# Kernel tuning notes

Hardware: AMD Instinct MI355X
Metric: run time of the kernel (lower is better)

Reference implementation:

```python
import jax, jax.numpy as jnp
import numpy as np
import math

N_LAYER = 3
D = 256
NH = 4
MULT = 128
N = MULT * D // NH  # 8192
VOCAB = 256
EPS = 1e-5
TWO_PI = 2.0 * math.pi


def _get_freqs(n, theta=2.0 ** 16):
    t = jnp.arange(0, n, dtype=jnp.float32)
    q = jnp.floor(t / 2.0) * 2.0  # quantize to pairs
    return 1.0 / (theta ** (q / n)) / TWO_PI  # [N]


def _ln(x):
    # LayerNorm over last dim, no affine
    mu = jnp.mean(x, axis=-1, keepdims=True)
    var = jnp.var(x, axis=-1, keepdims=True)
    return (x - mu) / jnp.sqrt(var + EPS)


def _rope(phases, v):
    # phases: [T, N] (cycles); v: [..., T, N]
    ph = (phases % 1.0) * TWO_PI
    c, s = jnp.cos(ph), jnp.sin(ph)
    v_rot = jnp.stack((-v[..., 1::2], v[..., ::2]), axis=-1).reshape(v.shape)
    return v * c + v_rot * s


def setup_inputs() -> dict:
    key = jax.random.key(0)
    ks = jax.random.split(key, 6)
    B, T = 1, 1024
    std = 0.02
    return {
        "idx": jax.random.randint(ks[0], (B, T), 0, VOCAB),
        "embed": jax.random.normal(ks[1], (VOCAB, D), jnp.float32) * std,
        "encoder": jax.random.normal(ks[2], (NH, D, N), jnp.float32) * std,
        "encoder_v": jax.random.normal(ks[3], (NH, D, N), jnp.float32) * std,
        "decoder": jax.random.normal(ks[4], (NH * N, D), jnp.float32) * std,
        "lm_head": jax.random.normal(ks[5], (D, VOCAB), jnp.float32) * std,
    }


def reference(idx, embed, encoder, encoder_v, decoder, lm_head):
    B, T = idx.shape
    freqs = _get_freqs(N)  # [N]
    phases = jnp.arange(T, dtype=jnp.float32)[:, None] * freqs[None, :]  # [T, N]
    # strict lower triangular causal mask (diagonal excluded)
    causal = jnp.tril(jnp.ones((T, T), dtype=jnp.bool_), k=-1)

    x = _ln(embed[idx])  # [B, T, D]
    for _ in range(N_LAYER):
        # encoder projection + ReLU sparsification: [B, nh, T, N]
        x_sparse = jax.nn.relu(jnp.einsum('btd,hdn->bhtn', x, encoder))
        # RoPE on Q (= K)
        qr = _rope(phases, x_sparse)
        # unnormalized bilinear causal attention (no softmax)
        scores = jnp.einsum('bhtn,bhsn->bhts', qr, qr)
        scores = jnp.where(causal, scores, 0.0)
        ykv = _ln(jnp.einsum('bhts,bsd->bhtd', scores, x))  # [B, nh, T, D]
        y_sparse = jax.nn.relu(jnp.einsum('bhtd,hdn->bhtn', ykv, encoder_v))
        xy = x_sparse * y_sparse  # [B, nh, T, N]
        # MLP decode: head-major flatten of (nh, N) matches decoder rows
        ymlp = jnp.einsum('bhtn,btd... wrong', xy) if False else (
            xy.transpose(0, 2, 1, 3).reshape(B, T, NH * N) @ decoder)  # [B, T, D]
        x = _ln(x + _ln(ymlp))
    logits = x @ lm_head  # [B, T, VOCAB]
    return logits
```

## Files before the change

### kernel.cpp

```cpp
#include <hip/hip_runtime.h>
#include <hip/hip_bf16.h>
#include <math.h>
#include <stdint.h>

#define T_SEQ 1024
#define D_DIM 256
#define NH_C 4
#define N_DIM 8192
#define VOCAB_C 256
#define NLAYER 3
#define TWO_PI_F 6.283185307179586f
#define KSPLIT_DEC 16
#define KSPLIT_SC 4

typedef __bf16 bf16x8 __attribute__((ext_vector_type(8)));
typedef float f32x4 __attribute__((ext_vector_type(4)));

__device__ __forceinline__ unsigned short f2bf(float f) {
  unsigned u = __builtin_bit_cast(unsigned, f);
  u += 0x7fffu + ((u >> 16) & 1u);
  return (unsigned short)(u >> 16);
}
__device__ __forceinline__ float bf2f(unsigned short h) {
  unsigned u = ((unsigned)h) << 16;
  return __builtin_bit_cast(float, u);
}
__device__ __forceinline__ unsigned pack2(float a, float b) {
  return (unsigned)f2bf(a) | ((unsigned)f2bf(b) << 16);
}

typedef __attribute__((address_space(3))) uint32_t lds_u32;
typedef __attribute__((address_space(1))) const uint32_t glob_u32;
__device__ __forceinline__ void gload_lds16(const void* g, void* l) {
  __builtin_amdgcn_global_load_lds(reinterpret_cast<glob_u32*>(reinterpret_cast<uintptr_t>(g)),
                                   reinterpret_cast<lds_u32*>(reinterpret_cast<uintptr_t>(l)), 16, 0,
                                   0);
}

__global__ void k_transpose(const float* __restrict__ src, unsigned short* __restrict__ dst,
                            int R, int C, long sB, long dB) {
  __shared__ float tile[32][33];
  const int b = blockIdx.z;
  src += (size_t)b * sB;
  dst += (size_t)b * dB;
  const int c0 = blockIdx.x * 32, r0 = blockIdx.y * 32;
  const int tx = threadIdx.x, ty = threadIdx.y;
#pragma unroll
  for (int i = 0; i < 32; i += 8)
    tile[ty + i][tx] = src[(size_t)(r0 + ty + i) * C + (c0 + tx)];
  __syncthreads();
#pragma unroll
  for (int i = 0; i < 32; i += 8)
    dst[(size_t)(c0 + ty + i) * R + (r0 + tx)] = f2bf(tile[tx][ty + i]);
}

__global__ void k_ropetab(unsigned* __restrict__ cs) {
  const int id = blockIdx.x * 256 + threadIdx.x;
  const int pair = id >> 10, t = id & 1023;
  const float freq = exp2f(-(float)pair * (1.0f / 256.0f)) * (1.0f / TWO_PI_F);
  float ph = (float)t * freq;
  ph -= floorf(ph);
  float s, c;
  __sincosf(ph * TWO_PI_F, &s, &c);
  cs[id] = pack2(c, s);
}

__device__ __forceinline__ void stats256(float4 v, float& mu, float& rs) {
  float s = v.x + v.y + v.z + v.w;
  float ss = v.x * v.x + v.y * v.y + v.z * v.z + v.w * v.w;
#pragma unroll
  for (int o = 1; o < 64; o <<= 1) { s += __shfl_xor(s, o); ss += __shfl_xor(ss, o); }
  mu = s * (1.0f / 256.0f);
  float var = ss * (1.0f / 256.0f) - mu * mu;
  rs = rsqrtf(var + 1e-5f);
}

__global__ void k_embed_ln(const int* __restrict__ idx, const float* __restrict__ embed,
                           float* __restrict__ x, unsigned short* __restrict__ xb,
                           unsigned short* __restrict__ xT) {
  const int t = blockIdx.x, lane = threadIdx.x;
  const float* row = embed + (size_t)idx[t] * D_DIM;
  float4 v = ((const float4*)row)[lane];
  float mu, rs;
  stats256(v, mu, rs);
  float4 o = make_float4((v.x - mu) * rs, (v.y - mu) * rs, (v.z - mu) * rs, (v.w - mu) * rs);
  ((float4*)(x + (size_t)t * D_DIM))[lane] = o;
  ((uint2*)(xb + (size_t)t * D_DIM))[lane] = make_uint2(pack2(o.x, o.y), pack2(o.z, o.w));
  const int d0 = lane * 4;
  xT[(size_t)(d0 + 0) * T_SEQ + t] = f2bf(o.x);
  xT[(size_t)(d0 + 1) * T_SEQ + t] = f2bf(o.y);
  xT[(size_t)(d0 + 2) * T_SEQ + t] = f2bf(o.z);
  xT[(size_t)(d0 + 3) * T_SEQ + t] = f2bf(o.w);
}

__global__ void k_ln_rows(const float* __restrict__ in, unsigned short* __restrict__ outb) {
  const int r = blockIdx.x, lane = threadIdx.x;
  float4 v = ((const float4*)(in + (size_t)r * D_DIM))[lane];
  float mu, rs;
  stats256(v, mu, rs);
  ((uint2*)(outb + (size_t)r * D_DIM))[lane] =
      make_uint2(pack2((v.x - mu) * rs, (v.y - mu) * rs), pack2((v.z - mu) * rs, (v.w - mu) * rs));
}

template <int NP>
__global__ void k_update_x(const float* __restrict__ ymlp, float* __restrict__ x,
                           unsigned short* __restrict__ xb, unsigned short* __restrict__ xT) {
  const int t = blockIdx.x, lane = threadIdx.x;
  float4 m = make_float4(0.f, 0.f, 0.f, 0.f);
#pragma unroll
  for (int pp = 0; pp < NP; ++pp) {
    float4 q = ((const float4*)(ymlp + (size_t)pp * T_SEQ * D_DIM + (size_t)t * D_DIM))[lane];
    m.x += q.x; m.y += q.y; m.z += q.z; m.w += q.w;
  }
  float mu1, rs1;
  stats256(m, mu1, rs1);
  float4 xv = ((const float4*)(x + (size_t)t * D_DIM))[lane];
  float4 z = make_float4(xv.x + (m.x - mu1) * rs1, xv.y + (m.y - mu1) * rs1,
                         xv.z + (m.z - mu1) * rs1, xv.w + (m.w - mu1) * rs1);
  float mu2, rs2;
  stats256(z, mu2, rs2);
  float4 o = make_float4((z.x - mu2) * rs2, (z.y - mu2) * rs2, (z.z - mu2) * rs2, (z.w - mu2) * rs2);
  ((float4*)(x + (size_t)t * D_DIM))[lane] = o;
  ((uint2*)(xb + (size_t)t * D_DIM))[lane] = make_uint2(pack2(o.x, o.y), pack2(o.z, o.w));
  const int d0 = lane * 4;
  xT[(size_t)(d0 + 0) * T_SEQ + t] = f2bf(o.x);
  xT[(size_t)(d0 + 1) * T_SEQ + t] = f2bf(o.y);
  xT[(size_t)(d0 + 2) * T_SEQ + t] = f2bf(o.z);
  xT[(size_t)(d0 + 3) * T_SEQ + t] = f2bf(o.w);
}

template <int NP>
__global__ void k_comb(const float* __restrict__ sp, unsigned short* __restrict__ sc) {
  const size_t gid = (size_t)blockIdx.x * 256 + threadIdx.x;
  const size_t e0 = gid * 8;
  const int s = (int)(e0 & (T_SEQ - 1));
  const int t = (int)((e0 >> 10) & (T_SEQ - 1));
  if (s >= t) return;
  const int h = (int)(e0 >> 20);
  float v[8] = {0.f, 0.f, 0.f, 0.f, 0.f, 0.f, 0.f, 0.f};
#pragma unroll
  for (int pp = 0; pp < NP; ++pp) {
    const float* a = sp + ((size_t)(h * NP + pp)) * T_SEQ * T_SEQ + (size_t)t * T_SEQ + s;
    float4 a0 = *(const float4*)a, a1 = *(const float4*)(a + 4);
    v[0] += a0.x; v[1] += a0.y; v[2] += a0.z; v[3] += a0.w;
    v[4] += a1.x; v[5] += a1.y; v[6] += a1.z; v[7] += a1.w;
  }
  unsigned short o[8];
#pragma unroll
  for (int j = 0; j < 8; ++j) o[j] = (s + j < t) ? f2bf(v[j]) : (unsigned short)0;
  *(uint4*)(sc + e0) = *(uint4*)o;
}

template <int MODE, int BM, int BN, bool TRI_A>
__global__ __launch_bounds__(256) void k_gemm(const unsigned short* __restrict__ A, long lda, long sAz,
                                              const unsigned short* __restrict__ B, long ldb, long sBz,
                                              void* __restrict__ Cv, long ldc, long sCz,
                                              const unsigned short* __restrict__ extra, long sEz,
                                              unsigned short* __restrict__ C2,
                                              const unsigned* __restrict__ ctab, int Ksize) {
  constexpr int MF = BM / 32;
  constexpr int NF = BN / 32;
  constexpr int BUFB = (BM + BN) * 128;

  const unsigned nbx = gridDim.x, nby = gridDim.y;
  const unsigned total = nbx * nby * gridDim.z;
  const unsigned lid = (blockIdx.z * nby + blockIdx.y) * nbx + blockIdx.x;
  const unsigned qq = total >> 3, rr = total & 7;
  const unsigned xcd = lid & 7, loc = lid >> 3;
  const unsigned wg = (xcd < rr ? xcd * (qq + 1) : rr * (qq + 1) + (xcd - rr) * qq) + loc;
  const int bx = wg % nbx;
  const int by = (wg / nbx) % nby;
  const int bz = wg / (nbx * nby);

  const int i0 = by * BM;
  const int j0 = bx * BN;
  if ((MODE == 2 || MODE == 6) && j0 >= i0 + BM) return;

  int zAB = bz, kbase = 0;
  if constexpr (MODE == 7) kbase = bz * Ksize;
  if constexpr (MODE == 6) { zAB = bz >> 2; kbase = (bz & (KSPLIT_SC - 1)) * Ksize; }
  A += (size_t)zAB * sAz;
  B += (size_t)zAB * sBz;
  float* Cf = (float*)Cv + (size_t)bz * sCz;
  unsigned short* Ch = (unsigned short*)Cv + (size_t)bz * sCz;
  unsigned short* C2h = C2 ? C2 + (size_t)bz * sCz : nullptr;
  const unsigned short* E = extra ? extra + (size_t)bz * sEz : nullptr;

  const int tid = threadIdx.x;
  const int lane = tid & 63, w = tid >> 6;
  const int wr = w >> 1, wc = w & 1;

  __shared__ __align__(16) char lds[2 * BUFB];

  f32x4 acc[MF][NF];
#pragma unroll
  for (int m = 0; m < MF; ++m)
#pragma unroll
    for (int n = 0; n < NF; ++n) acc[m][n] = f32x4{0.f, 0.f, 0.f, 0.f};

  const char* Abytes = (const char*)A;
  const char* Bbytes = (const char*)B;
  const size_t ldab = (size_t)((MODE == 7) ? N_DIM : lda) * 2;
  const size_t ldbb = (size_t)ldb * 2;
  const int lr = lane >> 3;
  const int scol = ((lane & 7) * 16) ^ (lr << 4);

  auto stage = [&](int buf, int kt) {
    const int kk = kbase + kt * 64;
    const char* Ag;
    if constexpr (MODE == 7) {
      Ag = Abytes +
           ((size_t)(kk >> 13) * ((size_t)T_SEQ * N_DIM) + (size_t)i0 * N_DIM + (kk & (N_DIM - 1))) * 2;
    } else {
      Ag = Abytes + ((size_t)i0 * lda + kk) * 2;
    }
    const char* Bg = Bbytes + ((size_t)j0 * ldb + kk) * 2;
    char* lb = lds + buf * BUFB;
#pragma unroll
    for (int it = 0; it < BM / 32; ++it) {
      const int r0 = (w + 4 * it) * 8;
      gload_lds16(Ag + (size_t)(r0 + lr) * ldab + scol, lb + r0 * 128);
    }
#pragma unroll
    for (int it = 0; it < BN / 32; ++it) {
      const int r0 = (w + 4 * it) * 8;
      gload_lds16(Bg + (size_t)(r0 + lr) * ldbb + scol, lb + BM * 128 + r0 * 128);
    }
  };

  const int ar = lane & 15;
  const int ko16 = (lane >> 4) * 16;
  const int swz = (lane & 7) << 4;

  auto compute = [&](const char* Ab) {
    const char* Bb = Ab + BM * 128;
    bf16x8 af[2][MF], bfr[2][NF];
#pragma unroll
    for (int kk = 0; kk < 2; ++kk) {
      const int koff = (kk * 64 + ko16) ^ swz;
#pragma unroll
      for (int m = 0; m < MF; ++m)
        af[kk][m] = *(const bf16x8*)(Ab + (size_t)(wr * (BM / 2) + m * 16 + ar) * 128 + koff);
#pragma unroll
      for (int n = 0; n < NF; ++n)
        bfr[kk][n] = *(const bf16x8*)(Bb + (size_t)(wc * (BN / 2) + n * 16 + ar) * 128 + koff);
    }
#pragma unroll
    for (int kk = 0; kk < 2; ++kk)
#pragma unroll
      for (int m = 0; m < MF; ++m)
#pragma unroll
        for (int n = 0; n < NF; ++n)
          acc[m][n] = __builtin_amdgcn_mfma_f32_16x16x32_bf16(af[kk][m], bfr[kk][n], acc[m][n], 0, 0, 0);
  };

  const int nt = TRI_A ? (i0 / 64 + BM / 64) : Ksize / 64;
  stage(0, 0);
  __syncthreads();
  int cur = 0;
  for (int t = 0; t < nt; ++t) {
    if (t + 1 < nt) stage(cur ^ 1, t + 1);
    compute(lds + cur * BUFB);
    __syncthreads();
    cur ^= 1;
  }

#pragma unroll
  for (int m = 0; m < MF; ++m) {
    const int row0 = i0 + wr * (BM / 2) + m * 16 + ((lane >> 4) << 2);
#pragma unroll
    for (int n = 0; n < NF; ++n) {
      const int col = j0 + wc * (BN / 2) + n * 16 + (lane & 15);
      f32x4 c = acc[m][n];
      if constexpr (MODE == 4) {
        const uint4 q = *(const uint4*)(ctab + (size_t)(col >> 1) * T_SEQ + row0);
        const unsigned qw[4] = {q.x, q.y, q.z, q.w};
        const float sgn = (lane & 1) ? 1.f : -1.f;
#pragma unroll
        for (int r = 0; r < 4; ++r) {
          const float v = fmaxf(c[r], 0.f);
          const float pv = __shfl_xor(v, 1);
          const float cc = bf2f((unsigned short)(qw[r] & 0xffffu));
          const float ss = bf2f((unsigned short)(qw[r] >> 16));
          Ch[(size_t)(row0 + r) * ldc + col] = f2bf(v);
          C2h[(size_t)(row0 + r) * ldc + col] = f2bf(v * cc + sgn * pv * ss);
        }
      } else {
#pragma unroll
        for (int r = 0; r < 4; ++r) {
          const int row = row0 + r;
          const float v = c[r];
          if constexpr (MODE == 0 || MODE == 6 || MODE == 7) {
            Cf[(size_t)row * ldc + col] = v;
          } else if constexpr (MODE == 2) {
            Ch[(size_t)row * ldc + col] = (col < row) ? f2bf(v) : (unsigned short)0;
          } else if constexpr (MODE == 3) {
            float g = bf2f(E[(size_t)row * ldc + col]);
            Ch[(size_t)row * ldc + col] = f2bf(fmaxf(v, 0.f) * g);
          }
        }
      }
    }
  }
}

extern "C" void kernel_launch(void* const* d_in, const int* in_sizes, int n_in,
                              void* d_out, int out_size, void* d_ws, size_t ws_size,
                              hipStream_t stream) {
  const int* idx = (const int*)d_in[0];
  const float* embed = (const float*)d_in[1];
  const float* enc = (const float*)d_in[2];
  const float* encv = (const float*)d_in[3];
  const float* dec = (const float*)d_in[4];
  const float* lmh = (const float*)d_in[5];
  float* out = (float*)d_out;

  char* p = (char*)d_ws;
  auto carve = [&](size_t bytes) -> void* {
    void* r = (void*)p;
    p += (bytes + 255) & ~(size_t)255;
    return r;
  };
  unsigned short* encT = (unsigned short*)carve((size_t)NH_C * N_DIM * D_DIM * 2);
  unsigned short* encvT = (unsigned short*)carve((size_t)NH_C * N_DIM * D_DIM * 2);
  unsigned short* decT = (unsigned short*)carve((size_t)D_DIM * NH_C * N_DIM * 2);
  unsigned short* lmT = (unsigned short*)carve((size_t)VOCAB_C * D_DIM * 2);
  float* x = (float*)carve((size_t)T_SEQ * D_DIM * 4);
  unsigned short* xb = (unsigned short*)carve((size_t)T_SEQ * D_DIM * 2);
  unsigned short* xT = (unsigned short*)carve((size_t)D_DIM * T_SEQ * 2);
  unsigned short* xs = (unsigned short*)carve((size_t)NH_C * T_SEQ * N_DIM * 2);
  unsigned short* qr = (unsigned short*)carve((size_t)NH_C * T_SEQ * N_DIM * 2);
  unsigned short* sc = (unsigned short*)carve((size_t)NH_C * T_SEQ * T_SEQ * 2);
  float* ykv = (float*)carve((size_t)NH_C * T_SEQ * D_DIM * 4);
  unsigned short* ykvln = (unsigned short*)carve((size_t)NH_C * T_SEQ * D_DIM * 2);
  float* ymlp = (float*)carve((size_t)KSPLIT_DEC * T_SEQ * D_DIM * 4);
  unsigned* cstab = (unsigned*)carve((size_t)(N_DIM / 2) * T_SEQ * 4);
  float* scf32 = (float*)carve((size_t)KSPLIT_SC * NH_C * T_SEQ * T_SEQ * 4);
  const bool split_ok = ((size_t)(p - (char*)d_ws) <= ws_size);

  const dim3 tb32(32, 8);
  k_transpose<<<dim3(N_DIM / 32, D_DIM / 32, NH_C), tb32, 0, stream>>>(
      enc, encT, D_DIM, N_DIM, (long)D_DIM * N_DIM, (long)N_DIM * D_DIM);
  k_transpose<<<dim3(N_DIM / 32, D_DIM / 32, NH_C), tb32, 0, stream>>>(
      encv, encvT, D_DIM, N_DIM, (long)D_DIM * N_DIM, (long)N_DIM * D_DIM);
  k_transpose<<<dim3(D_DIM / 32, (NH_C * N_DIM) / 32, 1), tb32, 0, stream>>>(
      dec, decT, NH_C * N_DIM, D_DIM, 0, 0);
  k_transpose<<<dim3(VOCAB_C / 32, D_DIM / 32, 1), tb32, 0, stream>>>(lmh, lmT, D_DIM, VOCAB_C, 0, 0);
  k_ropetab<<<((N_DIM / 2) * T_SEQ) / 256, 256, 0, stream>>>(cstab);
  k_embed_ln<<<T_SEQ, 64, 0, stream>>>(idx, embed, x, xb, xT);
  (void)hipMemsetAsync(sc, 0, (size_t)NH_C * T_SEQ * T_SEQ * 2, stream);

  for (int l = 0; l < NLAYER; ++l) {
    k_gemm<4, 128, 128, false><<<dim3(N_DIM / 128, T_SEQ / 128, NH_C), 256, 0, stream>>>(
        xb, D_DIM, 0, encT, D_DIM, (long)N_DIM * D_DIM, xs, N_DIM, (long)T_SEQ * N_DIM, nullptr, 0,
        qr, cstab, D_DIM);
    if (split_ok) {
      k_gemm<6, 128, 128, false>
          <<<dim3(T_SEQ / 128, T_SEQ / 128, KSPLIT_SC * NH_C), 256, 0, stream>>>(
              qr, N_DIM, (long)T_SEQ * N_DIM, qr, N_DIM, (long)T_SEQ * N_DIM, scf32, T_SEQ,
              (long)T_SEQ * T_SEQ, nullptr, 0, nullptr, nullptr, N_DIM / KSPLIT_SC);
      k_comb<KSPLIT_SC><<<(NH_C * T_SEQ * T_SEQ / 8) / 256, 256, 0, stream>>>(scf32, sc);
    } else {
      k_gemm<2, 128, 128, false><<<dim3(T_SEQ / 128, T_SEQ / 128, NH_C), 256, 0, stream>>>(
          qr, N_DIM, (long)T_SEQ * N_DIM, qr, N_DIM, (long)T_SEQ * N_DIM, sc, T_SEQ,
          (long)T_SEQ * T_SEQ, nullptr, 0, nullptr, nullptr, N_DIM);
    }
    k_gemm<0, 64, 64, true><<<dim3(D_DIM / 64, T_SEQ / 64, NH_C), 256, 0, stream>>>(
        sc, T_SEQ, (long)T_SEQ * T_SEQ, xT, T_SEQ, 0, ykv, D_DIM, (long)T_SEQ * D_DIM, nullptr, 0,
        nullptr, nullptr, T_SEQ);
    k_ln_rows<<<NH_C * T_SEQ, 64, 0, stream>>>(ykv, ykvln);
    k_gemm<3, 128, 128, false><<<dim3(N_DIM / 128, T_SEQ / 128, NH_C), 256, 0, stream>>>(
        ykvln, D_DIM, (long)T_SEQ * D_DIM, encvT, D_DIM, (long)N_DIM * D_DIM, qr, N_DIM,
        (long)T_SEQ * N_DIM, xs, (long)T_SEQ * N_DIM, nullptr, nullptr, D_DIM);
    k_gemm<7, 128, 64, false>
        <<<dim3(D_DIM / 64, T_SEQ / 128, KSPLIT_DEC), 256, 0, stream>>>(
            qr, N_DIM, 0, decT, (long)(NH_C * N_DIM), 0, ymlp, D_DIM, (long)T_SEQ * D_DIM,
            nullptr, 0, nullptr, nullptr, (NH_C * N_DIM) / KSPLIT_DEC);
    k_update_x<KSPLIT_DEC><<<T_SEQ, 64, 0, stream>>>(ymlp, x, xb, xT);
  }
  k_gemm<0, 64, 64, false><<<dim3(VOCAB_C / 64, T_SEQ / 64, 1), 256, 0, stream>>>(
      xb, D_DIM, 0, lmT, D_DIM, 0, out, VOCAB_C, 0, nullptr, 0, nullptr, nullptr, D_DIM);
}
```

Before: 745.1 us.

## Replace split-K score GEMM with triangular-indexed grid; retile decoder and swap block order

Drops the split-K fp32 score path and its combine kernel. Scores are now computed by a single 64x64-tile GEMM whose 1D grid enumerates only the lower-triangular tiles per head, mapping linear ids to (row, col) with a sqrt-based index. This removes the fp32 partial-score traffic and the extra launch, and avoids launching blocks that exit immediately. The encoder GEMMs now walk the row dimension fastest (SWAPXY) to change L2 reuse of weight tiles, and the decoder GEMM moves to 64x64 tiles for more blocks. Smaller tiles lower per-block reuse and the full K=8192 per tile may lengthen the critical path.

```diff
diff --git a/kernel.cpp b/kernel.cpp
--- a/kernel.cpp
+++ b/kernel.cpp
@@ -11,7 +11,6 @@
 #define NLAYER 3
 #define TWO_PI_F 6.283185307179586f
 #define KSPLIT_DEC 16
-#define KSPLIT_SC 4
 
 typedef __bf16 bf16x8 __attribute__((ext_vector_type(8)));
 typedef float f32x4 __attribute__((ext_vector_type(4)));
@@ -129,29 +128,7 @@
   xT[(size_t)(d0 + 3) * T_SEQ + t] = f2bf(o.w);
 }
 
-template <int NP>
-__global__ void k_comb(const float* __restrict__ sp, unsigned short* __restrict__ sc) {
-  const size_t gid = (size_t)blockIdx.x * 256 + threadIdx.x;
-  const size_t e0 = gid * 8;
-  const int s = (int)(e0 & (T_SEQ - 1));
-  const int t = (int)((e0 >> 10) & (T_SEQ - 1));
-  if (s >= t) return;
-  const int h = (int)(e0 >> 20);
-  float v[8] = {0.f, 0.f, 0.f, 0.f, 0.f, 0.f, 0.f, 0.f};
-#pragma unroll
-  for (int pp = 0; pp < NP; ++pp) {
-    const float* a = sp + ((size_t)(h * NP + pp)) * T_SEQ * T_SEQ + (size_t)t * T_SEQ + s;
-    float4 a0 = *(const float4*)a, a1 = *(const float4*)(a + 4);
-    v[0] += a0.x; v[1] += a0.y; v[2] += a0.z; v[3] += a0.w;
-    v[4] += a1.x; v[5] += a1.y; v[6] += a1.z; v[7] += a1.w;
-  }
-  unsigned short o[8];
-#pragma unroll
-  for (int j = 0; j < 8; ++j) o[j] = (s + j < t) ? f2bf(v[j]) : (unsigned short)0;
-  *(uint4*)(sc + e0) = *(uint4*)o;
-}
-
-template <int MODE, int BM, int BN, bool TRI_A>
+template <int MODE, int BM, int BN, bool TRI_A, bool SWAPXY>
 __global__ __launch_bounds__(256) void k_gemm(const unsigned short* __restrict__ A, long lda, long sAz,
                                               const unsigned short* __restrict__ B, long ldb, long sBz,
                                               void* __restrict__ Cv, long ldc, long sCz,
@@ -168,19 +145,34 @@
   const unsigned qq = total >> 3, rr = total & 7;
   const unsigned xcd = lid & 7, loc = lid >> 3;
   const unsigned wg = (xcd < rr ? xcd * (qq + 1) : rr * (qq + 1) + (xcd - rr) * qq) + loc;
-  const int bx = wg % nbx;
-  const int by = (wg / nbx) % nby;
-  const int bz = wg / (nbx * nby);
+
+  int bx, by, bz;
+  if constexpr (MODE == 2) {
+    constexpr int TPH = (T_SEQ / BM) * (T_SEQ / BM + 1) / 2;
+    bz = wg / TPH;
+    const int tt = wg % TPH;
+    by = (int)((sqrtf(8.0f * (float)tt + 1.0f) - 1.0f) * 0.5f);
+    if (by > T_SEQ / BM - 1) by = T_SEQ / BM - 1;
+    while ((by + 1) * (by + 2) / 2 <= tt) ++by;
+    while (by * (by + 1) / 2 > tt) --by;
+    bx = tt - by * (by + 1) / 2;
+  } else if constexpr (SWAPXY) {
+    by = wg % nby;
+    bx = (wg / nby) % nbx;
+    bz = wg / (nbx * nby);
+  } else {
+    bx = wg % nbx;
+    by = (wg / nbx) % nby;
+    bz = wg / (nbx * nby);
+  }
 
   const int i0 = by * BM;
   const int j0 = bx * BN;
-  if ((MODE == 2 || MODE == 6) && j0 >= i0 + BM) return;
-
-  int zAB = bz, kbase = 0;
+
+  int kbase = 0;
   if constexpr (MODE == 7) kbase = bz * Ksize;
-  if constexpr (MODE == 6) { zAB = bz >> 2; kbase = (bz & (KSPLIT_SC - 1)) * Ksize; }
-  A += (size_t)zAB * sAz;
-  B += (size_t)zAB * sBz;
+  A += (size_t)bz * sAz;
+  B += (size_t)bz * sBz;
   float* Cf = (float*)Cv + (size_t)bz * sCz;
   unsigned short* Ch = (unsigned short*)Cv + (size_t)bz * sCz;
   unsigned short* C2h = C2 ? C2 + (size_t)bz * sCz : nullptr;
@@ -290,7 +282,7 @@
         for (int r = 0; r < 4; ++r) {
           const int row = row0 + r;
           const float v = c[r];
-          if constexpr (MODE == 0 || MODE == 6 || MODE == 7) {
+          if constexpr (MODE == 0 || MODE == 7) {
             Cf[(size_t)row * ldc + col] = v;
           } else if constexpr (MODE == 2) {
             Ch[(size_t)row * ldc + col] = (col < row) ? f2bf(v) : (unsigned short)0;
@@ -335,8 +327,6 @@
   unsigned short* ykvln = (unsigned short*)carve((size_t)NH_C * T_SEQ * D_DIM * 2);
   float* ymlp = (float*)carve((size_t)KSPLIT_DEC * T_SEQ * D_DIM * 4);
   unsigned* cstab = (unsigned*)carve((size_t)(N_DIM / 2) * T_SEQ * 4);
-  float* scf32 = (float*)carve((size_t)KSPLIT_SC * NH_C * T_SEQ * T_SEQ * 4);
-  const bool split_ok = ((size_t)(p - (char*)d_ws) <= ws_size);
 
   const dim3 tb32(32, 8);
   k_transpose<<<dim3(N_DIM / 32, D_DIM / 32, NH_C), tb32, 0, stream>>>(
@@ -351,33 +341,26 @@
   (void)hipMemsetAsync(sc, 0, (size_t)NH_C * T_SEQ * T_SEQ * 2, stream);
 
   for (int l = 0; l < NLAYER; ++l) {
-    k_gemm<4, 128, 128, false><<<dim3(N_DIM / 128, T_SEQ / 128, NH_C), 256, 0, stream>>>(
+    k_gemm<4, 128, 128, false, true><<<dim3(N_DIM / 128, T_SEQ / 128, NH_C), 256, 0, stream>>>(
         xb, D_DIM, 0, encT, D_DIM, (long)N_DIM * D_DIM, xs, N_DIM, (long)T_SEQ * N_DIM, nullptr, 0,
         qr, cstab, D_DIM);
-    if (split_ok) {
-      k_gemm<6, 128, 128, false>
-          <<<dim3(T_SEQ / 128, T_SEQ / 128, KSPLIT_SC * NH_C), 256, 0, stream>>>(
-              qr, N_DIM, (long)T_SEQ * N_DIM, qr, N_DIM, (long)T_SEQ * N_DIM, scf32, T_SEQ,
-              (long)T_SEQ * T_SEQ, nullptr, 0, nullptr, nullptr, N_DIM / KSPLIT_SC);
-      k_comb<KSPLIT_SC><<<(NH_C * T_SEQ * T_SEQ / 8) / 256, 256, 0, stream>>>(scf32, sc);
-    } else {
-      k_gemm<2, 128, 128, false><<<dim3(T_SEQ / 128, T_SEQ / 128, NH_C), 256, 0, stream>>>(
-          qr, N_DIM, (long)T_SEQ * N_DIM, qr, N_DIM, (long)T_SEQ * N_DIM, sc, T_SEQ,
-          (long)T_SEQ * T_SEQ, nullptr, 0, nullptr, nullptr, N_DIM);
-    }
-    k_gemm<0, 64, 64, true><<<dim3(D_DIM / 64, T_SEQ / 64, NH_C), 256, 0, stream>>>(
+    k_gemm<2, 64, 64, false, false>
+        <<<dim3(NH_C * (T_SEQ / 64) * (T_SEQ / 64 + 1) / 2, 1, 1), 256, 0, stream>>>(
+            qr, N_DIM, (long)T_SEQ * N_DIM, qr, N_DIM, (long)T_SEQ * N_DIM, sc, T_SEQ,
+            (long)T_SEQ * T_SEQ, nullptr, 0, nullptr, nullptr, N_DIM);
+    k_gemm<0, 64, 64, true, false><<<dim3(D_DIM / 64, T_SEQ / 64, NH_C), 256, 0, stream>>>(
         sc, T_SEQ, (long)T_SEQ * T_SEQ, xT, T_SEQ, 0, ykv, D_DIM, (long)T_SEQ * D_DIM, nullptr, 0,
         nullptr, nullptr, T_SEQ);
     k_ln_rows<<<NH_C * T_SEQ, 64, 0, stream>>>(ykv, ykvln);
-    k_gemm<3, 128, 128, false><<<dim3(N_DIM / 128, T_SEQ / 128, NH_C), 256, 0, stream>>>(
+    k_gemm<3, 128, 128, false, true><<<dim3(N_DIM / 128, T_SEQ / 128, NH_C), 256, 0, stream>>>(
         ykvln, D_DIM, (long)T_SEQ * D_DIM, encvT, D_DIM, (long)N_DIM * D_DIM, qr, N_DIM,
         (long)T_SEQ * N_DIM, xs, (long)T_SEQ * N_DIM, nullptr, nullptr, D_DIM);
-    k_gemm<7, 128, 64, false>
-        <<<dim3(D_DIM / 64, T_SEQ / 128, KSPLIT_DEC), 256, 0, stream>>>(
+    k_gemm<7, 64, 64, false, false>
+        <<<dim3(D_DIM / 64, T_SEQ / 64, KSPLIT_DEC), 256, 0, stream>>>(
             qr, N_DIM, 0, decT, (long)(NH_C * N_DIM), 0, ymlp, D_DIM, (long)T_SEQ * D_DIM,
             nullptr, 0, nullptr, nullptr, (NH_C * N_DIM) / KSPLIT_DEC);
     k_update_x<KSPLIT_DEC><<<T_SEQ, 64, 0, stream>>>(ymlp, x, xb, xT);
   }
-  k_gemm<0, 64, 64, false><<<dim3(VOCAB_C / 64, T_SEQ / 64, 1), 256, 0, stream>>>(
+  k_gemm<0, 64, 64, false, false><<<dim3(VOCAB_C / 64, T_SEQ / 64, 1), 256, 0, stream>>>(
       xb, D_DIM, 0, lmT, D_DIM, 0, out, VOCAB_C, 0, nullptr, 0, nullptr, nullptr, D_DIM);
 }
```

Result: faster. 676.0 us (-9.3%).

## Launch only lower-triangular score tiles and retune split-K and tile rasterization

Applied to the files above, without the earlier changes.

The causal score GEMM now launches a 1D grid covering only lower-triangular tiles, mapping each linear id to (row, col) with a sqrt-based triangular index. Before, it launched the full square grid and upper-triangle blocks returned early. Split-K for the scores drops from 4 to 2, and the decoder split-K rises from 16 to 32 with 128x128 tiles. The encoder GEMMs get a swapped x/y rasterization so that consecutive workgroups share the same weight column tile, which aims at better cache reuse. Together these change occupancy, the size of the fp32 partial buffers and the reduction traffic, and each could help or hurt.

```diff
diff --git a/kernel.cpp b/kernel.cpp
--- a/kernel.cpp
+++ b/kernel.cpp
@@ -10,8 +10,8 @@
 #define VOCAB_C 256
 #define NLAYER 3
 #define TWO_PI_F 6.283185307179586f
-#define KSPLIT_DEC 16
-#define KSPLIT_SC 4
+#define KSPLIT_DEC 32
+#define KSPLIT_SC 2
 
 typedef __bf16 bf16x8 __attribute__((ext_vector_type(8)));
 typedef float f32x4 __attribute__((ext_vector_type(4)));
@@ -151,7 +151,7 @@
   *(uint4*)(sc + e0) = *(uint4*)o;
 }
 
-template <int MODE, int BM, int BN, bool TRI_A>
+template <int MODE, int BM, int BN, bool TRI_A, bool SWAPXY>
 __global__ __launch_bounds__(256) void k_gemm(const unsigned short* __restrict__ A, long lda, long sAz,
                                               const unsigned short* __restrict__ B, long ldb, long sBz,
                                               void* __restrict__ Cv, long ldc, long sCz,
@@ -168,17 +168,41 @@
   const unsigned qq = total >> 3, rr = total & 7;
   const unsigned xcd = lid & 7, loc = lid >> 3;
   const unsigned wg = (xcd < rr ? xcd * (qq + 1) : rr * (qq + 1) + (xcd - rr) * qq) + loc;
-  const int bx = wg % nbx;
-  const int by = (wg / nbx) % nby;
-  const int bz = wg / (nbx * nby);
+
+  int bx, by, bz, zAB, kbase = 0;
+  if constexpr (MODE == 2 || MODE == 6) {
+    constexpr int NRT = T_SEQ / BM;
+    constexpr int TPH = NRT * (NRT + 1) / 2;
+    const int zz = wg / TPH;
+    const int tt = wg % TPH;
+    by = (int)((sqrtf(8.0f * (float)tt + 1.0f) - 1.0f) * 0.5f);
+    if (by > NRT - 1) by = NRT - 1;
+    while ((by + 1) * (by + 2) / 2 <= tt) ++by;
+    while (by * (by + 1) / 2 > tt) --by;
+    bx = tt - by * (by + 1) / 2;
+    bz = zz;
+    if constexpr (MODE == 6) {
+      zAB = zz >> 1;
+      kbase = (zz & 1) * Ksize;
+    } else {
+      zAB = zz;
+    }
+  } else if constexpr (SWAPXY) {
+    by = wg % nby;
+    bx = (wg / nby) % nbx;
+    bz = wg / (nbx * nby);
+    zAB = bz;
+  } else {
+    bx = wg % nbx;
+    by = (wg / nbx) % nby;
+    bz = wg / (nbx * nby);
+    zAB = bz;
+  }
+  if constexpr (MODE == 7) kbase = bz * Ksize;
 
   const int i0 = by * BM;
   const int j0 = bx * BN;
-  if ((MODE == 2 || MODE == 6) && j0 >= i0 + BM) return;
-
-  int zAB = bz, kbase = 0;
-  if constexpr (MODE == 7) kbase = bz * Ksize;
-  if constexpr (MODE == 6) { zAB = bz >> 2; kbase = (bz & (KSPLIT_SC - 1)) * Ksize; }
+
   A += (size_t)zAB * sAz;
   B += (size_t)zAB * sBz;
   float* Cf = (float*)Cv + (size_t)bz * sCz;
@@ -351,33 +375,34 @@
   (void)hipMemsetAsync(sc, 0, (size_t)NH_C * T_SEQ * T_SEQ * 2, stream);
 
   for (int l = 0; l < NLAYER; ++l) {
-    k_gemm<4, 128, 128, false><<<dim3(N_DIM / 128, T_SEQ / 128, NH_C), 256, 0, stream>>>(
+    k_gemm<4, 128, 128, false, true><<<dim3(N_DIM / 128, T_SEQ / 128, NH_C), 256, 0, stream>>>(
         xb, D_DIM, 0, encT, D_DIM, (long)N_DIM * D_DIM, xs, N_DIM, (long)T_SEQ * N_DIM, nullptr, 0,
         qr, cstab, D_DIM);
     if (split_ok) {
-      k_gemm<6, 128, 128, false>
-          <<<dim3(T_SEQ / 128, T_SEQ / 128, KSPLIT_SC * NH_C), 256, 0, stream>>>(
+      k_gemm<6, 128, 128, false, false>
+          <<<dim3(KSPLIT_SC * NH_C * (T_SEQ / 128) * (T_SEQ / 128 + 1) / 2, 1, 1), 256, 0, stream>>>(
               qr, N_DIM, (long)T_SEQ * N_DIM, qr, N_DIM, (long)T_SEQ * N_DIM, scf32, T_SEQ,
               (long)T_SEQ * T_SEQ, nullptr, 0, nullptr, nullptr, N_DIM / KSPLIT_SC);
       k_comb<KSPLIT_SC><<<(NH_C * T_SEQ * T_SEQ / 8) / 256, 256, 0, stream>>>(scf32, sc);
     } else {
-      k_gemm<2, 128, 128, false><<<dim3(T_SEQ / 128, T_SEQ / 128, NH_C), 256, 0, stream>>>(
-          qr, N_DIM, (long)T_SEQ * N_DIM, qr, N_DIM, (long)T_SEQ * N_DIM, sc, T_SEQ,
-          (long)T_SEQ * T_SEQ, nullptr, 0, nullptr, nullptr, N_DIM);
-    }
-    k_gemm<0, 64, 64, true><<<dim3(D_DIM / 64, T_SEQ / 64, NH_C), 256, 0, stream>>>(
+      k_gemm<2, 64, 64, false, false>
+          <<<dim3(NH_C * (T_SEQ / 64) * (T_SEQ / 64 + 1) / 2, 1, 1), 256, 0, stream>>>(
+              qr, N_DIM, (long)T_SEQ * N_DIM, qr, N_DIM, (long)T_SEQ * N_DIM, sc, T_SEQ,
+              (long)T_SEQ * T_SEQ, nullptr, 0, nullptr, nullptr, N_DIM);
+    }
+    k_gemm<0, 64, 64, true, false><<<dim3(D_DIM / 64, T_SEQ / 64, NH_C), 256, 0, stream>>>(
         sc, T_SEQ, (long)T_SEQ * T_SEQ, xT, T_SEQ, 0, ykv, D_DIM, (long)T_SEQ * D_DIM, nullptr, 0,
         nullptr, nullptr, T_SEQ);
     k_ln_rows<<<NH_C * T_SEQ, 64, 0, stream>>>(ykv, ykvln);
-    k_gemm<3, 128, 128, false><<<dim3(N_DIM / 128, T_SEQ / 128, NH_C), 256, 0, stream>>>(
+    k_gemm<3, 128, 128, false, true><<<dim3(N_DIM / 128, T_SEQ / 128, NH_C), 256, 0, stream>>>(
         ykvln, D_DIM, (long)T_SEQ * D_DIM, encvT, D_DIM, (long)N_DIM * D_DIM, qr, N_DIM,
         (long)T_SEQ * N_DIM, xs, (long)T_SEQ * N_DIM, nullptr, nullptr, D_DIM);
-    k_gemm<7, 128, 64, false>
-        <<<dim3(D_DIM / 64, T_SEQ / 128, KSPLIT_DEC), 256, 0, stream>>>(
+    k_gemm<7, 128, 128, false, false>
+        <<<dim3(D_DIM / 128, T_SEQ / 128, KSPLIT_DEC), 256, 0, stream>>>(
             qr, N_DIM, 0, decT, (long)(NH_C * N_DIM), 0, ymlp, D_DIM, (long)T_SEQ * D_DIM,
             nullptr, 0, nullptr, nullptr, (NH_C * N_DIM) / KSPLIT_DEC);
     k_update_x<KSPLIT_DEC><<<T_SEQ, 64, 0, stream>>>(ymlp, x, xb, xT);
   }
-  k_gemm<0, 64, 64, false><<<dim3(VOCAB_C / 64, T_SEQ / 64, 1), 256, 0, stream>>>(
+  k_gemm<0, 64, 64, false, false><<<dim3(VOCAB_C / 64, T_SEQ / 64, 1), 256, 0, stream>>>(
       xb, D_DIM, 0, lmT, D_DIM, 0, out, VOCAB_C, 0, nullptr, 0, nullptr, nullptr, D_DIM);
 }
```

After: 667.1 us. -10.5%, faster.
